# Performance work log

Measured on AMD Instinct MI355X. Metric: run time of the kernel, lower is better.

## Reference

```python
import jax, jax.numpy as jnp
import numpy as np

N_EMBED = 1024
HEAD_SIZE = 64
BLOCK_SIZE = 2048


def setup_inputs() -> dict:
    key = jax.random.key(0)
    kx, kk, kv = jax.random.split(key, 3)
    x = jax.random.normal(kx, (8, 2048, N_EMBED), dtype=jnp.float32)
    # nn.Linear(n_embed, head_size, bias=False): weight [head_size, n_embed]
    scale = 1.0 / np.sqrt(N_EMBED)
    W_k = jax.random.uniform(kk, (HEAD_SIZE, N_EMBED), dtype=jnp.float32, minval=-scale, maxval=scale)
    W_v = jax.random.uniform(kv, (HEAD_SIZE, N_EMBED), dtype=jnp.float32, minval=-scale, maxval=scale)
    return {"x": x, "W_k": W_k, "W_v": W_v}


def reference(x, W_k, W_v):
    # Faithful to source: q = self.key(x) (query projection is unused in the original forward)
    T = x.shape[1]
    k = jnp.einsum('btc,hc->bth', x, W_k)   # [B,T,H]
    q = k                                    # source bug: q uses key projection
    wei = jnp.einsum('bth,bsh->bts', q, k) * (HEAD_SIZE ** -0.5)  # [B,T,T]
    causal = jnp.tril(jnp.ones((T, T), dtype=bool))
    wei = jnp.where(causal, wei, -jnp.inf)
    wei = jax.nn.softmax(wei, axis=-1)
    v = jnp.einsum('btc,hc->bth', x, W_v)
    out = jnp.einsum('bts,bsh->bth', wei, v)
    return out
```

## Files before the change

### kernel.cpp

```cpp
#include <hip/hip_runtime.h>


typedef __bf16 bf16;
typedef __bf16 bf16x4 __attribute__((ext_vector_type(4)));
typedef __bf16 bf16x8 __attribute__((ext_vector_type(8)));
typedef float  floatx4 __attribute__((ext_vector_type(4)));

#define T_LEN 2048
#define HEAD  64
#define CEMB  1024

static __device__ __forceinline__ bf16x8 cvt2(float4 a, float4 b) {
    bf16x8 r;
    r[0] = (bf16)a.x; r[1] = (bf16)a.y; r[2] = (bf16)a.z; r[3] = (bf16)a.w;
    r[4] = (bf16)b.x; r[5] = (bf16)b.y; r[6] = (bf16)b.z; r[7] = (bf16)b.w;
    return r;
}

__global__ __launch_bounds__(256) void wconv_kernel(const float* __restrict__ Wk,
                                                    const float* __restrict__ Wv,
                                                    bf16* __restrict__ Wb) {
    int i = (blockIdx.x * 256 + threadIdx.x) * 4;
    const float* src = (i < 64 * 1024) ? (Wk + i) : (Wv + (i - 64 * 1024));
    float4 f = *(const float4*)src;
    bf16x4 v;
    v[0] = (bf16)f.x; v[1] = (bf16)f.y; v[2] = (bf16)f.z; v[3] = (bf16)f.w;
    *(bf16x4*)&Wb[i] = v;
}

__global__ __launch_bounds__(256) void proj_kernel(const float* __restrict__ x,
                                                   const bf16* __restrict__ Wb,
                                                   bf16* __restrict__ Kbuf,
                                                   bf16* __restrict__ Vt) {
    __shared__ __align__(16) bf16 As[2][32][72];
    __shared__ __align__(16) bf16 Bs[2][128][72];

    const int tid  = threadIdx.x;
    const int wave = tid >> 6;
    const int lane = tid & 63;
    const int quad = lane >> 4;
    const int low  = lane & 15;

    const long row0 = (long)blockIdx.x * 32;

    const int a_row = tid >> 3;
    const int a_col = (tid & 7) * 8;
    const int b_row = tid >> 1;
    const int b_col = (tid & 1) * 32;

    const float* abase = x + (row0 + a_row) * CEMB + a_col;
    const bf16*  bbase = Wb + b_row * CEMB + b_col;

    const int strip = wave & 1;
    const int nhalf = wave >> 1;
    const int nq    = nhalf * 4;

    floatx4 acc[4];
#pragma unroll
    for (int i = 0; i < 4; ++i) acc[i] = (floatx4){0.f, 0.f, 0.f, 0.f};

    float4 apf[2][2];
    bf16x8 bpf[2][4];

    apf[0][0] = ((const float4*)abase)[0];
    apf[0][1] = ((const float4*)abase)[1];
#pragma unroll
    for (int i = 0; i < 4; ++i) bpf[0][i] = *(const bf16x8*)(bbase + 8 * i);
    *(bf16x8*)&As[0][a_row][a_col] = cvt2(apf[0][0], apf[0][1]);
#pragma unroll
    for (int i = 0; i < 4; ++i) *(bf16x8*)&Bs[0][b_row][b_col + 8 * i] = bpf[0][i];
    apf[1][0] = ((const float4*)(abase + 64))[0];
    apf[1][1] = ((const float4*)(abase + 64))[1];
#pragma unroll
    for (int i = 0; i < 4; ++i) bpf[1][i] = *(const bf16x8*)(bbase + 64 + 8 * i);
    __syncthreads();

    int buf = 0;
    for (int s = 0; s < 16; ++s) {
        if (s < 15) {
            const int q  = (s + 1) & 1;
            const int nb = buf ^ 1;
            *(bf16x8*)&As[nb][a_row][a_col] = cvt2(apf[q][0], apf[q][1]);
#pragma unroll
            for (int i = 0; i < 4; ++i) *(bf16x8*)&Bs[nb][b_row][b_col + 8 * i] = bpf[q][i];
        }
        if (s < 14) {
            const int q  = s & 1;
            const int k0 = (s + 2) * 64;
            apf[q][0] = ((const float4*)(abase + k0))[0];
            apf[q][1] = ((const float4*)(abase + k0))[1];
#pragma unroll
            for (int i = 0; i < 4; ++i) bpf[q][i] = *(const bf16x8*)(bbase + k0 + 8 * i);
        }
#pragma unroll
        for (int ks = 0; ks < 2; ++ks) {
            bf16x8 afrag = *(const bf16x8*)&As[buf][strip * 16 + low][ks * 32 + quad * 8];
#pragma unroll
            for (int i = 0; i < 4; ++i) {
                bf16x8 bfrag = *(const bf16x8*)&Bs[buf][(nq + i) * 16 + low][ks * 32 + quad * 8];
                acc[i] = __builtin_amdgcn_mfma_f32_16x16x32_bf16(afrag, bfrag, acc[i], 0, 0, 0);
            }
        }
        if (s < 15) {
            __syncthreads();
            buf ^= 1;
        }
    }

    __syncthreads();
    bf16* Ek = (bf16*)&Bs[0][0][0];
    bf16* Ev = (bf16*)&Bs[1][0][0];
    if (nhalf == 0) {
#pragma unroll
        for (int i = 0; i < 4; ++i)
#pragma unroll
            for (int r = 0; r < 4; ++r)
                Ek[(strip * 16 + quad * 4 + r) * 72 + i * 16 + low] = (bf16)acc[i][r];
    } else {
#pragma unroll
        for (int i = 0; i < 4; ++i)
#pragma unroll
            for (int r = 0; r < 4; ++r)
                Ev[(i * 16 + low) * 36 + strip * 16 + quad * 4 + r] = (bf16)acc[i][r];
    }
    __syncthreads();

    const long bidx  = row0 >> 11;
    const int  tloc0 = (int)(row0 & 2047);
    {
        const int t  = tid >> 3;
        const int h0 = (tid & 7) * 8;
        *(bf16x8*)&Kbuf[(bidx * T_LEN + tloc0 + t) * HEAD + h0] = *(const bf16x8*)&Ek[t * 72 + h0];
    }
    {
        const int h  = tid >> 2;
        const int t0 = (tid & 3) * 8;
        *(bf16x8*)&Vt[(bidx * HEAD + h) * T_LEN + tloc0 + t0] = *(const bf16x8*)&Ev[h * 36 + t0];
    }
}

__global__ __launch_bounds__(256) void attn_kernel(const bf16* __restrict__ Kbuf,
                                                   const bf16* __restrict__ Vt,
                                                   bf16* __restrict__ Opart,
                                                   float* __restrict__ lpart) {
    __shared__ __align__(16) bf16 Ks[2][64][72];
    __shared__ __align__(16) bf16 Vs[2][64][72];
    __shared__ __align__(16) bf16 Ps[4][16][72];

    const int tid  = threadIdx.x;
    const int wave = tid >> 6;
    const int lane = tid & 63;
    const int quad = lane >> 4;
    const int low  = lane & 15;

    const int c  = blockIdx.x & 3;
    const int qb = (blockIdx.x >> 2) & 31;
    const int b  = blockIdx.x >> 7;

    const bf16* kbase = Kbuf + (long)b * T_LEN * HEAD;
    const bf16* vbase = Vt + (long)b * HEAD * T_LEN;

    const bf16* qrow = kbase + (qb * 64 + wave * 16 + low) * HEAD + quad * 8;
    const bf16x8 qf0 = *(const bf16x8*)(qrow);
    const bf16x8 qf1 = *(const bf16x8*)(qrow + 32);

    bf16x8 ones;
#pragma unroll
    for (int i = 0; i < 8; ++i) ones[i] = (bf16)1.0f;

    floatx4 o[4], ol;
#pragma unroll
    for (int nt = 0; nt < 4; ++nt) o[nt] = (floatx4){0.f, 0.f, 0.f, 0.f};
    ol = (floatx4){0.f, 0.f, 0.f, 0.f};

    const int s_row = tid >> 2;
    const int s_col = (tid & 3) * 16;
    const bf16* ksrc = kbase + s_row * HEAD + s_col;
    const bf16* vsrc = vbase + (long)s_row * T_LEN + s_col;

    if (c <= qb) {
        float4 kpf0 = *(const float4*)(ksrc + c * 4096);
        float4 kpf1 = *(const float4*)(ksrc + c * 4096 + 8);
        float4 vpf0 = *(const float4*)(vsrc + c * 64);
        float4 vpf1 = *(const float4*)(vsrc + c * 64 + 8);
        *(float4*)&Ks[0][s_row][s_col]     = kpf0;
        *(float4*)&Ks[0][s_row][s_col + 8] = kpf1;
        *(float4*)&Vs[0][s_row][s_col]     = vpf0;
        *(float4*)&Vs[0][s_row][s_col + 8] = vpf1;
        __syncthreads();

        int buf = 0;
        for (int j = c; j <= qb; j += 4) {
            const bool more = (j + 4 <= qb);
            if (more) {
                kpf0 = *(const float4*)(ksrc + (j + 4) * 4096);
                kpf1 = *(const float4*)(ksrc + (j + 4) * 4096 + 8);
                vpf0 = *(const float4*)(vsrc + (j + 4) * 64);
                vpf1 = *(const float4*)(vsrc + (j + 4) * 64 + 8);
            }

            floatx4 s_[4];
#pragma unroll
            for (int nt = 0; nt < 4; ++nt) {
                bf16x8 kf0 = *(const bf16x8*)&Ks[buf][nt * 16 + low][quad * 8];
                bf16x8 kf1 = *(const bf16x8*)&Ks[buf][nt * 16 + low][32 + quad * 8];
                floatx4 z = (floatx4){0.f, 0.f, 0.f, 0.f};
                z = __builtin_amdgcn_mfma_f32_16x16x32_bf16(qf0, kf0, z, 0, 0, 0);
                z = __builtin_amdgcn_mfma_f32_16x16x32_bf16(qf1, kf1, z, 0, 0, 0);
                s_[nt] = z;
            }

            const bool diag = (j == qb);
#pragma unroll
            for (int nt = 0; nt < 4; ++nt) {
#pragma unroll
                for (int r = 0; r < 4; ++r) {
                    float p = __builtin_amdgcn_exp2f(s_[nt][r] * 0.180336880f);
                    if (diag && (nt * 16 + low) > (wave * 16 + quad * 4 + r)) p = 0.f;
                    Ps[wave][quad * 4 + r][nt * 16 + low] = (bf16)p;
                }
            }

            bf16x8 pf0 = *(const bf16x8*)&Ps[wave][low][quad * 8];
            bf16x8 pf1 = *(const bf16x8*)&Ps[wave][low][32 + quad * 8];
#pragma unroll
            for (int nt = 0; nt < 4; ++nt) {
                bf16x8 vf0 = *(const bf16x8*)&Vs[buf][nt * 16 + low][quad * 8];
                bf16x8 vf1 = *(const bf16x8*)&Vs[buf][nt * 16 + low][32 + quad * 8];
                o[nt] = __builtin_amdgcn_mfma_f32_16x16x32_bf16(pf0, vf0, o[nt], 0, 0, 0);
                o[nt] = __builtin_amdgcn_mfma_f32_16x16x32_bf16(pf1, vf1, o[nt], 0, 0, 0);
            }
            ol = __builtin_amdgcn_mfma_f32_16x16x32_bf16(pf0, ones, ol, 0, 0, 0);
            ol = __builtin_amdgcn_mfma_f32_16x16x32_bf16(pf1, ones, ol, 0, 0, 0);

            if (more) {
                const int nb = buf ^ 1;
                *(float4*)&Ks[nb][s_row][s_col]     = kpf0;
                *(float4*)&Ks[nb][s_row][s_col + 8] = kpf1;
                *(float4*)&Vs[nb][s_row][s_col]     = vpf0;
                *(float4*)&Vs[nb][s_row][s_col + 8] = vpf1;
                __syncthreads();
                buf = nb;
            }
        }
    }

    __syncthreads();
    bf16* Eo = (bf16*)&Ks[0][0][0];
#pragma unroll
    for (int nt = 0; nt < 4; ++nt)
#pragma unroll
        for (int r = 0; r < 4; ++r)
            Eo[(wave * 16 + quad * 4 + r) * 72 + nt * 16 + low] = (bf16)o[nt][r];
    __syncthreads();
    {
        const int row  = tid >> 2;
        const int col0 = (tid & 3) * 16;
        bf16* ob = Opart + (long)blockIdx.x * 4096 + row * 64 + col0;
        *(bf16x8*)(ob)     = *(const bf16x8*)&Eo[row * 72 + col0];
        *(bf16x8*)(ob + 8) = *(const bf16x8*)&Eo[row * 72 + col0 + 8];
    }
    if (low == 0) {
#pragma unroll
        for (int r = 0; r < 4; ++r)
            lpart[(long)blockIdx.x * 64 + wave * 16 + quad * 4 + r] = ol[r];
    }
}

__global__ __launch_bounds__(256) void attn_combine(const bf16* __restrict__ Opart,
                                                    const float* __restrict__ lpart,
                                                    float* __restrict__ out) {
    const int tile = blockIdx.x;
    const int tid  = threadIdx.x;
    const int row  = tid >> 2;
    const int col0 = (tid & 3) * 16;

    const bf16*  ob = Opart + (long)tile * 4 * 4096 + row * 64 + col0;
    const float* lb = lpart + (long)tile * 4 * 64 + row;

    float l = lb[0] + lb[64] + lb[128] + lb[192];
    float rl = 1.0f / l;

    float s[16];
#pragma unroll
    for (int i = 0; i < 16; ++i) s[i] = 0.f;
#pragma unroll
    for (int ch = 0; ch < 4; ++ch) {
        bf16x8 u0 = *(const bf16x8*)(ob + ch * 4096);
        bf16x8 u1 = *(const bf16x8*)(ob + ch * 4096 + 8);
#pragma unroll
        for (int i = 0; i < 8; ++i) { s[i] += (float)u0[i]; s[8 + i] += (float)u1[i]; }
    }
    float4* op = (float4*)(out + (long)tile * 4096 + row * 64 + col0);
#pragma unroll
    for (int v = 0; v < 4; ++v) {
        float4 w;
        w.x = s[v * 4 + 0] * rl; w.y = s[v * 4 + 1] * rl;
        w.z = s[v * 4 + 2] * rl; w.w = s[v * 4 + 3] * rl;
        op[v] = w;
    }
}

extern "C" void kernel_launch(void* const* d_in, const int* in_sizes, int n_in,
                              void* d_out, int out_size, void* d_ws, size_t ws_size,
                              hipStream_t stream) {
    const float* x  = (const float*)d_in[0];
    const float* Wk = (const float*)d_in[1];
    const float* Wv = (const float*)d_in[2];
    float* out = (float*)d_out;

    char* ws = (char*)d_ws;
    bf16*  Wb    = (bf16*)ws;
    bf16*  Kbuf  = (bf16*)(ws + (1 << 20));
    bf16*  Vt    = (bf16*)(ws + (3 << 20));
    bf16*  Opart = (bf16*)(ws + (5 << 20));
    float* lpart = (float*)(ws + (13 << 20));

    wconv_kernel<<<128, 256, 0, stream>>>(Wk, Wv, Wb);
    proj_kernel<<<512, 256, 0, stream>>>(x, Wb, Kbuf, Vt);
    attn_kernel<<<1024, 256, 0, stream>>>(Kbuf, Vt, Opart, lpart);
    attn_combine<<<256, 256, 0, stream>>>(Opart, lpart, out);
}
```

Before: 129.5 us.

## Use direct global-to-LDS loads with XOR swizzle for weight and K/V tiles

Replaces register-staged global loads and LDS stores of the weight tiles in the projection kernel, and of the K/V tiles in the attention kernel, with global_load_lds DMA into unpadded LDS buffers. An XOR swizzle on 16-byte chunks replaces the row padding to avoid bank conflicts. This aims to cut register pressure and VALU/LDS-store instructions and to let loads overlap compute. Separately, the combine kernel is split across four times as many blocks with narrower per-thread work. The risk is correctness of the swizzle and the wave-to-LDS address mapping, plus synchronisation of the asynchronous LDS writes.

Measured after the change: 128.3 us. About the same (-0.9%).

```diff
diff --git a/kernel.cpp b/kernel.cpp
--- a/kernel.cpp
+++ b/kernel.cpp
@@ -15,6 +15,13 @@
     r[0] = (bf16)a.x; r[1] = (bf16)a.y; r[2] = (bf16)a.z; r[3] = (bf16)a.w;
     r[4] = (bf16)b.x; r[5] = (bf16)b.y; r[6] = (bf16)b.z; r[7] = (bf16)b.w;
     return r;
+}
+
+static __device__ __forceinline__ void gload_lds16(const void* g, void* l) {
+    __builtin_amdgcn_global_load_lds(
+        (const __attribute__((address_space(1))) unsigned int*)(unsigned long long)g,
+        (__attribute__((address_space(3))) unsigned int*)(unsigned long long)l,
+        16, 0, 0);
 }
 
 __global__ __launch_bounds__(256) void wconv_kernel(const float* __restrict__ Wk,
@@ -33,7 +40,7 @@
                                                    bf16* __restrict__ Kbuf,
                                                    bf16* __restrict__ Vt) {
     __shared__ __align__(16) bf16 As[2][32][72];
-    __shared__ __align__(16) bf16 Bs[2][128][72];
+    __shared__ __align__(16) bf16 Bs[2][128][64];
 
     const int tid  = threadIdx.x;
     const int wave = tid >> 6;
@@ -45,11 +52,13 @@
 
     const int a_row = tid >> 3;
     const int a_col = (tid & 7) * 8;
-    const int b_row = tid >> 1;
-    const int b_col = (tid & 1) * 32;
-
     const float* abase = x + (row0 + a_row) * CEMB + a_col;
-    const bf16*  bbase = Wb + b_row * CEMB + b_col;
+
+    const int brow = tid >> 3;
+    const int cbp  = (tid & 7) * 16;
+    const int bsw  = cbp ^ ((brow & 7) << 4);
+    const char* bsrc0 = (const char*)Wb + (long)brow * (CEMB * 2) + bsw;
+    char* bdst = (char*)&Bs[0][0][0] + wave * 1024;
 
     const int strip = wave & 1;
     const int nhalf = wave >> 1;
@@ -60,21 +69,18 @@
     for (int i = 0; i < 4; ++i) acc[i] = (floatx4){0.f, 0.f, 0.f, 0.f};
 
     float4 apf[2][2];
-    bf16x8 bpf[2][4];
 
     apf[0][0] = ((const float4*)abase)[0];
     apf[0][1] = ((const float4*)abase)[1];
 #pragma unroll
-    for (int i = 0; i < 4; ++i) bpf[0][i] = *(const bf16x8*)(bbase + 8 * i);
+    for (int r = 0; r < 4; ++r)
+        gload_lds16(bsrc0 + (long)r * 65536, bdst + r * 4096);
     *(bf16x8*)&As[0][a_row][a_col] = cvt2(apf[0][0], apf[0][1]);
-#pragma unroll
-    for (int i = 0; i < 4; ++i) *(bf16x8*)&Bs[0][b_row][b_col + 8 * i] = bpf[0][i];
     apf[1][0] = ((const float4*)(abase + 64))[0];
     apf[1][1] = ((const float4*)(abase + 64))[1];
-#pragma unroll
-    for (int i = 0; i < 4; ++i) bpf[1][i] = *(const bf16x8*)(bbase + 64 + 8 * i);
-    __syncthreads();
-
+    __syncthreads();
+
+    const int bswz = (low & 7) << 4;
     int buf = 0;
     for (int s = 0; s < 16; ++s) {
         if (s < 15) {
@@ -82,22 +88,24 @@
             const int nb = buf ^ 1;
             *(bf16x8*)&As[nb][a_row][a_col] = cvt2(apf[q][0], apf[q][1]);
 #pragma unroll
-            for (int i = 0; i < 4; ++i) *(bf16x8*)&Bs[nb][b_row][b_col + 8 * i] = bpf[q][i];
+            for (int r = 0; r < 4; ++r)
+                gload_lds16(bsrc0 + (long)r * 65536 + (s + 1) * 128,
+                            bdst + nb * 16384 + r * 4096);
         }
         if (s < 14) {
             const int q  = s & 1;
             const int k0 = (s + 2) * 64;
             apf[q][0] = ((const float4*)(abase + k0))[0];
             apf[q][1] = ((const float4*)(abase + k0))[1];
-#pragma unroll
-            for (int i = 0; i < 4; ++i) bpf[q][i] = *(const bf16x8*)(bbase + k0 + 8 * i);
-        }
+        }
+        const char* bsl = (const char*)&Bs[buf][0][0];
 #pragma unroll
         for (int ks = 0; ks < 2; ++ks) {
             bf16x8 afrag = *(const bf16x8*)&As[buf][strip * 16 + low][ks * 32 + quad * 8];
+            const int cb = (ks * 64 + quad * 16) ^ bswz;
 #pragma unroll
             for (int i = 0; i < 4; ++i) {
-                bf16x8 bfrag = *(const bf16x8*)&Bs[buf][(nq + i) * 16 + low][ks * 32 + quad * 8];
+                bf16x8 bfrag = *(const bf16x8*)(bsl + ((nq + i) * 16 + low) * 128 + cb);
                 acc[i] = __builtin_amdgcn_mfma_f32_16x16x32_bf16(afrag, bfrag, acc[i], 0, 0, 0);
             }
         }
@@ -143,8 +151,8 @@
                                                    const bf16* __restrict__ Vt,
                                                    bf16* __restrict__ Opart,
                                                    float* __restrict__ lpart) {
-    __shared__ __align__(16) bf16 Ks[2][64][72];
-    __shared__ __align__(16) bf16 Vs[2][64][72];
+    __shared__ __align__(16) bf16 Ks[2][64][64];
+    __shared__ __align__(16) bf16 Vs[2][64][64];
     __shared__ __align__(16) bf16 Ps[4][16][72];
 
     const int tid  = threadIdx.x;
@@ -173,37 +181,47 @@
     for (int nt = 0; nt < 4; ++nt) o[nt] = (floatx4){0.f, 0.f, 0.f, 0.f};
     ol = (floatx4){0.f, 0.f, 0.f, 0.f};
 
-    const int s_row = tid >> 2;
-    const int s_col = (tid & 3) * 16;
-    const bf16* ksrc = kbase + s_row * HEAD + s_col;
-    const bf16* vsrc = vbase + (long)s_row * T_LEN + s_col;
+    const int srow = tid >> 3;
+    const int cbp  = (tid & 7) * 16;
+    const int ssw  = cbp ^ ((srow & 7) << 4);
+    const char* ksrc0 = (const char*)kbase + (long)srow * 128  + ssw;
+    const char* vsrc0 = (const char*)vbase + (long)srow * 4096 + ssw;
+    char* kdst = (char*)&Ks[0][0][0] + wave * 1024;
+    char* vdst = (char*)&Vs[0][0][0] + wave * 1024;
+
+    const int sw  = (low & 7) << 4;
+    const int cb0 = (quad * 16) ^ sw;
+    const int cb1 = (64 + quad * 16) ^ sw;
 
     if (c <= qb) {
-        float4 kpf0 = *(const float4*)(ksrc + c * 4096);
-        float4 kpf1 = *(const float4*)(ksrc + c * 4096 + 8);
-        float4 vpf0 = *(const float4*)(vsrc + c * 64);
-        float4 vpf1 = *(const float4*)(vsrc + c * 64 + 8);
-        *(float4*)&Ks[0][s_row][s_col]     = kpf0;
-        *(float4*)&Ks[0][s_row][s_col + 8] = kpf1;
-        *(float4*)&Vs[0][s_row][s_col]     = vpf0;
-        *(float4*)&Vs[0][s_row][s_col + 8] = vpf1;
+#pragma unroll
+        for (int r = 0; r < 2; ++r) {
+            gload_lds16(ksrc0 + (long)c * 8192 + r * 4096, kdst + r * 4096);
+            gload_lds16(vsrc0 + (long)c * 128 + (long)r * 131072, vdst + r * 4096);
+        }
         __syncthreads();
 
         int buf = 0;
         for (int j = c; j <= qb; j += 4) {
             const bool more = (j + 4 <= qb);
             if (more) {
-                kpf0 = *(const float4*)(ksrc + (j + 4) * 4096);
-                kpf1 = *(const float4*)(ksrc + (j + 4) * 4096 + 8);
-                vpf0 = *(const float4*)(vsrc + (j + 4) * 64);
-                vpf1 = *(const float4*)(vsrc + (j + 4) * 64 + 8);
-            }
+                const int nb = buf ^ 1;
+#pragma unroll
+                for (int r = 0; r < 2; ++r) {
+                    gload_lds16(ksrc0 + (long)(j + 4) * 8192 + r * 4096,
+                                kdst + nb * 8192 + r * 4096);
+                    gload_lds16(vsrc0 + (long)(j + 4) * 128 + (long)r * 131072,
+                                vdst + nb * 8192 + r * 4096);
+                }
+            }
+            const char* ksl = (const char*)&Ks[buf][0][0];
+            const char* vsl = (const char*)&Vs[buf][0][0];
 
             floatx4 s_[4];
 #pragma unroll
             for (int nt = 0; nt < 4; ++nt) {
-                bf16x8 kf0 = *(const bf16x8*)&Ks[buf][nt * 16 + low][quad * 8];
-                bf16x8 kf1 = *(const bf16x8*)&Ks[buf][nt * 16 + low][32 + quad * 8];
+                bf16x8 kf0 = *(const bf16x8*)(ksl + (nt * 16 + low) * 128 + cb0);
+                bf16x8 kf1 = *(const bf16x8*)(ksl + (nt * 16 + low) * 128 + cb1);
                 floatx4 z = (floatx4){0.f, 0.f, 0.f, 0.f};
                 z = __builtin_amdgcn_mfma_f32_16x16x32_bf16(qf0, kf0, z, 0, 0, 0);
                 z = __builtin_amdgcn_mfma_f32_16x16x32_bf16(qf1, kf1, z, 0, 0, 0);
@@ -225,8 +243,8 @@
             bf16x8 pf1 = *(const bf16x8*)&Ps[wave][low][32 + quad * 8];
 #pragma unroll
             for (int nt = 0; nt < 4; ++nt) {
-                bf16x8 vf0 = *(const bf16x8*)&Vs[buf][nt * 16 + low][quad * 8];
-                bf16x8 vf1 = *(const bf16x8*)&Vs[buf][nt * 16 + low][32 + quad * 8];
+                bf16x8 vf0 = *(const bf16x8*)(vsl + (nt * 16 + low) * 128 + cb0);
+                bf16x8 vf1 = *(const bf16x8*)(vsl + (nt * 16 + low) * 128 + cb1);
                 o[nt] = __builtin_amdgcn_mfma_f32_16x16x32_bf16(pf0, vf0, o[nt], 0, 0, 0);
                 o[nt] = __builtin_amdgcn_mfma_f32_16x16x32_bf16(pf1, vf1, o[nt], 0, 0, 0);
             }
@@ -234,13 +252,8 @@
             ol = __builtin_amdgcn_mfma_f32_16x16x32_bf16(pf1, ones, ol, 0, 0, 0);
 
             if (more) {
-                const int nb = buf ^ 1;
-                *(float4*)&Ks[nb][s_row][s_col]     = kpf0;
-                *(float4*)&Ks[nb][s_row][s_col + 8] = kpf1;
-                *(float4*)&Vs[nb][s_row][s_col]     = vpf0;
-                *(float4*)&Vs[nb][s_row][s_col + 8] = vpf1;
                 __syncthreads();
-                buf = nb;
+                buf ^= 1;
             }
         }
     }
@@ -270,10 +283,11 @@
 __global__ __launch_bounds__(256) void attn_combine(const bf16* __restrict__ Opart,
                                                     const float* __restrict__ lpart,
                                                     float* __restrict__ out) {
-    const int tile = blockIdx.x;
+    const int tile = blockIdx.x >> 2;
+    const int rg   = blockIdx.x & 3;
     const int tid  = threadIdx.x;
-    const int row  = tid >> 2;
-    const int col0 = (tid & 3) * 16;
+    const int row  = rg * 16 + (tid >> 4);
+    const int col0 = (tid & 15) * 4;
 
     const bf16*  ob = Opart + (long)tile * 4 * 4096 + row * 64 + col0;
     const float* lb = lpart + (long)tile * 4 * 64 + row;
@@ -281,24 +295,16 @@
     float l = lb[0] + lb[64] + lb[128] + lb[192];
     float rl = 1.0f / l;
 
-    float s[16];
-#pragma unroll
-    for (int i = 0; i < 16; ++i) s[i] = 0.f;
+    float s[4] = {0.f, 0.f, 0.f, 0.f};
 #pragma unroll
     for (int ch = 0; ch < 4; ++ch) {
-        bf16x8 u0 = *(const bf16x8*)(ob + ch * 4096);
-        bf16x8 u1 = *(const bf16x8*)(ob + ch * 4096 + 8);
-#pragma unroll
-        for (int i = 0; i < 8; ++i) { s[i] += (float)u0[i]; s[8 + i] += (float)u1[i]; }
-    }
-    float4* op = (float4*)(out + (long)tile * 4096 + row * 64 + col0);
-#pragma unroll
-    for (int v = 0; v < 4; ++v) {
-        float4 w;
-        w.x = s[v * 4 + 0] * rl; w.y = s[v * 4 + 1] * rl;
-        w.z = s[v * 4 + 2] * rl; w.w = s[v * 4 + 3] * rl;
-        op[v] = w;
-    }
+        bf16x4 u = *(const bf16x4*)(ob + ch * 4096);
+#pragma unroll
+        for (int i = 0; i < 4; ++i) s[i] += (float)u[i];
+    }
+    float4 w;
+    w.x = s[0] * rl; w.y = s[1] * rl; w.z = s[2] * rl; w.w = s[3] * rl;
+    *(float4*)(out + (long)tile * 4096 + row * 64 + col0) = w;
 }
 
 extern "C" void kernel_launch(void* const* d_in, const int* in_sizes, int n_in,
@@ -319,5 +325,5 @@
     wconv_kernel<<<128, 256, 0, stream>>>(Wk, Wv, Wb);
     proj_kernel<<<512, 256, 0, stream>>>(x, Wb, Kbuf, Vt);
     attn_kernel<<<1024, 256, 0, stream>>>(Kbuf, Vt, Opart, lpart);
-    attn_combine<<<256, 256, 0, stream>>>(Opart, lpart, out);
-}
+    attn_combine<<<1024, 256, 0, stream>>>(Opart, lpart, out);
+}
```
